# Performance work log

Hardware: AMD Instinct MI355X
Metric: run time of the kernel (lower is better)

## Reference

```python
import jax, jax.numpy as jnp
import numpy as np

T, Q, D, NH, L = 6, 300, 256, 8, 4
DH = D // NH
PC, PT = 2, 1
WT = T - 1
P = PC + WT * PT
DFF = 1024
SHAPES = [(128, 128), (64, 64), (32, 32), (16, 16)]
S_PER_FRAME = sum(h * w for h, w in SHAPES)


def _layer_norm(x, g, b, eps=1e-5):
    mu = jnp.mean(x, -1, keepdims=True)
    v = jnp.mean(jnp.square(x - mu), -1, keepdims=True)
    return (x - mu) * jax.lax.rsqrt(v + eps) * g + b


def _bilinear(vlh, loc, frame_pt, Hl, Wl):
    # vlh: [NH, T*Hl*Wl, DH]; loc: [TQ, NH, P, 2] normalized; frame_pt: np [TQ, P] int32
    x = loc[..., 0] * Wl - 0.5
    y = loc[..., 1] * Hl - 0.5
    x0 = jnp.floor(x)
    y0 = jnp.floor(y)
    fx = x - x0
    fy = y - y0
    x0 = x0.astype(jnp.int32)
    y0 = y0.astype(jnp.int32)
    fbase = (frame_pt[:, None, :] * np.int32(Hl * Wl)).astype(np.int32)  # [TQ,1,P]
    acc = 0.0
    for dy, wy in ((0, 1.0 - fy), (1, fy)):
        for dx, wx in ((0, 1.0 - fx), (1, fx)):
            xi = x0 + dx
            yi = y0 + dy
            ok = (xi >= 0) & (xi < Wl) & (yi >= 0) & (yi < Hl)
            idx = fbase + jnp.clip(yi, 0, Hl - 1) * Wl + jnp.clip(xi, 0, Wl - 1)  # [TQ,NH,P]
            g = jax.vmap(lambda v, i: v[i], in_axes=(0, 1), out_axes=0)(vlh, idx)  # [NH,TQ,P,DH]
            w = wy * wx * ok  # [TQ,NH,P]
            acc = acc + g * jnp.transpose(w, (1, 0, 2))[..., None]
    return acc  # [NH,TQ,P,DH]


def _forward(src, tgt_masks, query_pos, reference_points, src_valid_ratios,
             Wq, bq, Wk, bk, Wv, bv, Wo, bo, norm2_g, norm2_b,
             Wval, bval, Woff, boff, Watt, batt, Wout, bout, norm1_g, norm1_b,
             W1, b1, W2, b2, norm3_g, norm3_b,
             src_spatial_shapes, src_level_start_index):
    shapes = np.asarray(src_spatial_shapes)
    # ---- self-attention across frames (seq=T, batch=Q, as in nn.MultiheadAttention) ----
    qk_in = tgt_masks + query_pos  # [T,Q,D]
    qh = (qk_in @ Wq.T + bq).reshape(T, Q, NH, DH)
    kh = (qk_in @ Wk.T + bk).reshape(T, Q, NH, DH)
    vh = (tgt_masks @ Wv.T + bv).reshape(T, Q, NH, DH)
    logits = jnp.einsum('iqhd,jqhd->qhij', qh, kh) * (1.0 / np.sqrt(DH))
    attn = jax.nn.softmax(logits, -1)
    sa = jnp.einsum('qhij,jqhd->iqhd', attn, vh).reshape(T, Q, D) @ Wo.T + bo
    tgt = _layer_norm(tgt_masks + sa, norm2_g, norm2_b)  # [T,Q,D]

    tgt = tgt.reshape(T * Q, D)
    query = tgt + query_pos.reshape(T * Q, D)

    # ---- current-frame and temporal (same-instance) reference points ----
    ref = reference_points.reshape(T * Q, 2)
    vr0 = src_valid_ratios[0]  # [L,2]
    ref_curr = ref[:, None, :] * vr0[None]  # [TQ,L,2]
    others = np.array([[f for f in range(T) if f != t] for t in range(T)], np.int32)  # [T,WT]
    ref_oth = reference_points[others]  # [T,WT,Q,2]
    ref_oth = jnp.transpose(ref_oth, (0, 2, 1, 3)).reshape(T * Q, WT, 2)
    ref_temp = ref_oth[:, :, None, :] * vr0[None, None]  # [TQ,WT,L,2]

    fid = np.repeat(np.arange(T, dtype=np.int32), Q)  # [TQ]
    oth_fid = np.repeat(others, Q, axis=0)  # [TQ,WT]
    frame_pt = np.concatenate([np.tile(fid[:, None], (1, PC)), oth_fid], axis=1).astype(np.int32)  # [TQ,P]

    # ---- temporal multi-scale deformable cross-attention ----
    value = (src[0] @ Wval.T + bval).reshape(-1, NH, DH)  # [T*S,NH,DH]
    off = (query @ Woff.T + boff).reshape(T * Q, NH, L, P, 2)
    att = jax.nn.softmax((query @ Watt.T + batt).reshape(T * Q, NH, L * P), -1)
    att = att.reshape(T * Q, NH, L, P)

    out = jnp.zeros((T * Q, NH, DH), src.dtype)
    start = 0
    for l in range(L):
        Hl, Wl = int(shapes[l, 0]), int(shapes[l, 1])
        n = T * Hl * Wl
        vlh = value[start:start + n].transpose(1, 0, 2)  # [NH, T*Hl*Wl, DH]
        start += n
        bc = jnp.tile(ref_curr[:, l][:, None, :], (1, PC, 1))  # [TQ,PC,2]
        bt = ref_temp[:, :, l, :]  # [TQ,WT,2]
        base = jnp.concatenate([bc, bt], 1)[:, None]  # [TQ,1,P,2]
        loc = base + off[:, :, l] / jnp.array([Wl, Hl], jnp.float32)  # [TQ,NH,P,2]
        sampled = _bilinear(vlh, loc, frame_pt, Hl, Wl)  # [NH,TQ,P,DH]
        out = out + jnp.einsum('nqpd,qnp->qnd', sampled, att[:, :, l])
    cross = out.reshape(T * Q, D) @ Wout.T + bout
    tgt = _layer_norm(tgt + cross, norm1_g, norm1_b)

    # ---- FFN ----
    h = jax.nn.relu(tgt @ W1.T + b1)
    tgt = _layer_norm(tgt + h @ W2.T + b2, norm3_g, norm3_b)
    return tgt.reshape(T, Q, D)


def setup_inputs() -> dict:
    key = jax.random.key(0)
    ki = iter(jax.random.split(key, 48))

    def rn(shape, s=1.0):
        return jax.random.normal(next(ki), shape, jnp.float32) * s

    return {
        'src': rn((1, T * S_PER_FRAME, D)),
        'tgt_masks': rn((T, Q, D)),
        'query_pos': rn((T, Q, D), 0.5),
        'reference_points': jax.random.uniform(next(ki), (T, Q, 2), jnp.float32, 0.25, 0.75),
        'src_valid_ratios': jax.random.uniform(next(ki), (T, L, 2), jnp.float32, 0.9, 1.0),
        'src_spatial_shapes': jnp.array(SHAPES, jnp.int32),
        'src_level_start_index': jnp.array(np.cumsum([0] + [T * h * w for h, w in SHAPES[:-1]]), jnp.int32),
        'Wq': rn((D, D), 0.02), 'bq': jnp.zeros((D,)),
        'Wk': rn((D, D), 0.02), 'bk': jnp.zeros((D,)),
        'Wv': rn((D, D), 0.02), 'bv': jnp.zeros((D,)),
        'Wo': rn((D, D), 0.02), 'bo': jnp.zeros((D,)),
        'norm2_g': jnp.ones((D,)), 'norm2_b': jnp.zeros((D,)),
        'Wval': rn((D, D), 0.02), 'bval': jnp.zeros((D,)),
        'Woff': rn((NH * L * P * 2, D), 0.01), 'boff': rn((NH * L * P * 2,), 0.1),
        'Watt': rn((NH * L * P, D), 0.01), 'batt': jnp.zeros((NH * L * P,)),
        'Wout': rn((D, D), 0.02), 'bout': jnp.zeros((D,)),
        'norm1_g': jnp.ones((D,)), 'norm1_b': jnp.zeros((D,)),
        'W1': rn((DFF, D), 0.02), 'b1': jnp.zeros((DFF,)),
        'W2': rn((D, DFF), 0.02), 'b2': jnp.zeros((D,)),
        'norm3_g': jnp.ones((D,)), 'norm3_b': jnp.zeros((D,)),
    }


def reference(src, tgt_masks, query_pos, reference_points, src_valid_ratios,
              src_spatial_shapes, src_level_start_index,
              Wq, bq, Wk, bk, Wv, bv, Wo, bo, norm2_g, norm2_b,
              Wval, bval, Woff, boff, Watt, batt, Wout, bout, norm1_g, norm1_b,
              W1, b1, W2, b2, norm3_g, norm3_b):
    return _forward(src, tgt_masks, query_pos, reference_points, src_valid_ratios,
                    Wq, bq, Wk, bk, Wv, bv, Wo, bo, norm2_g, norm2_b,
                    Wval, bval, Woff, boff, Watt, batt, Wout, bout, norm1_g, norm1_b,
                    W1, b1, W2, b2, norm3_g, norm3_b,
                    src_spatial_shapes, src_level_start_index)
```

## Files before the change

kernel.cpp:

```cpp
#include <hip/hip_runtime.h>
#include <hip/hip_bf16.h>

#define T_ 6
#define Q_ 300
#define TQ 1800
#define D_ 256
#define NH_ 8
#define DH_ 32
#define L_ 4
#define P_ 7
#define DFF_ 1024
#define NV 130560
#define VBLK 255

#define OW_VAL 0
#define OW_Q   65536
#define OW_K   131072
#define OW_V   196608
#define OW_O   262144
#define OW_OUT 327680
#define OW_OFF 393216
#define OW_ATT 507904
#define OW_1   565248
#define OW_2   827392
#define OW_TOT 1089536

typedef __attribute__((ext_vector_type(8))) short bf16x8;
typedef __attribute__((ext_vector_type(4))) float f32x4;
typedef __attribute__((ext_vector_type(8))) unsigned short u16x8;
typedef __attribute__((ext_vector_type(4))) unsigned short u16x4;

__device__ inline float bf2f(unsigned short s) {
    union { unsigned u; float f; } v; v.u = ((unsigned)s) << 16;
    return v.f;
}
__device__ inline unsigned short f2b_rn(float f) {
    __hip_bfloat16 h = __float2bfloat16(f);
    union { __hip_bfloat16 h; unsigned short u; } c; c.h = h; return c.u;
}

__global__ __launch_bounds__(256) void wcvt_kernel(
    const float* __restrict__ s0, const float* __restrict__ s1,
    const float* __restrict__ s2, const float* __restrict__ s3,
    const float* __restrict__ s4, const float* __restrict__ s5,
    const float* __restrict__ s6, const float* __restrict__ s7,
    const float* __restrict__ s8, const float* __restrict__ s9,
    unsigned short* __restrict__ dst)
{
    int idx4 = blockIdx.x * blockDim.x + threadIdx.x;
    const int total4 = OW_TOT / 4;
    for (; idx4 < total4; idx4 += gridDim.x * blockDim.x) {
        int e = idx4 * 4;
        const float* s; int off;
        if      (e < OW_Q)   { s = s0; off = e; }
        else if (e < OW_K)   { s = s1; off = e - OW_Q; }
        else if (e < OW_V)   { s = s2; off = e - OW_K; }
        else if (e < OW_O)   { s = s3; off = e - OW_V; }
        else if (e < OW_OUT) { s = s4; off = e - OW_O; }
        else if (e < OW_OFF) { s = s5; off = e - OW_OUT; }
        else if (e < OW_ATT) { s = s6; off = e - OW_OFF; }
        else if (e < OW_1)   { s = s7; off = e - OW_ATT; }
        else if (e < OW_2)   { s = s8; off = e - OW_1; }
        else                 { s = s9; off = e - OW_2; }
        f32x4 v = *(const f32x4*)(s + off);
        u16x4 o;
#pragma unroll
        for (int j = 0; j < 4; j++) o[j] = f2b_rn(v[j]);
        *(u16x4*)(dst + e) = o;
    }
}

__global__ __launch_bounds__(512) void vgemm_kernel(
    const float* __restrict__ A, const unsigned short* __restrict__ wbf,
    const float* __restrict__ bias, unsigned short* __restrict__ out)
{
    __shared__ unsigned short Ws[256 * 256];
    __shared__ float As[2][128 * 32];

    int tid = threadIdx.x;
    int wave = tid >> 6, lane = tid & 63;
    int r = lane & 15, g = lane >> 4;
    int rs = r & 7;
    int base_m = blockIdx.x * 512;

#pragma unroll
    for (int j = 0; j < 16; j++) {
        int o = wave * 16 + j;
        int col = o * 2 + (lane >> 5);
        int slot = lane & 31;
        const unsigned short* s =
            wbf + OW_VAL + (size_t)col * 256 + (size_t)((slot ^ (col & 7)) * 8);
        __builtin_amdgcn_global_load_lds(
            (const __attribute__((address_space(1))) void*)s,
            (__attribute__((address_space(3))) void*)&Ws[o * 512], 16, 0, 0);
    }

#define DMA_A(tile, ks, b) do { \
        int o_ = wave * 2; \
        int ro_ = o_ * 8 + (lane >> 3); \
        int kg_ = (lane & 7) ^ (lane >> 3); \
        const float* s0_ = A + (size_t)(base_m + (tile) * 128 + ro_) * 256 + (ks) * 32 + kg_ * 4; \
        const float* s1_ = s0_ + 8 * 256; \
        __builtin_amdgcn_global_load_lds( \
            (const __attribute__((address_space(1))) void*)s0_, \
            (__attribute__((address_space(3))) void*)&As[b][o_ * 256], 16, 0, 0); \
        __builtin_amdgcn_global_load_lds( \
            (const __attribute__((address_space(1))) void*)s1_, \
            (__attribute__((address_space(3))) void*)&As[b][(o_ + 1) * 256], 16, 0, 0); \
    } while (0)

    DMA_A(0, 0, 0);
    DMA_A(0, 1, 1);

    int wm = wave >> 2, wn = wave & 3;
    f32x4 acc[4][4] = {};

    for (int p = 0; p < 32; ++p) {
        if (p == 31) { asm volatile("s_waitcnt vmcnt(0)" ::: "memory"); }
        else         { asm volatile("s_waitcnt vmcnt(2)" ::: "memory"); }
        __builtin_amdgcn_s_barrier();
        __builtin_amdgcn_sched_barrier(0);

        int tile = p >> 3, ks = p & 7, b = p & 1;

        {
            bf16x8 af[4];
#pragma unroll
            for (int mi = 0; mi < 4; mi++) {
                int row_ = wm * 64 + mi * 16 + r;
                f32x4 lo_ = *(const f32x4*)&As[b][row_ * 32 + (((g * 2) ^ rs) << 2)];
                f32x4 hi_ = *(const f32x4*)&As[b][row_ * 32 + (((g * 2 + 1) ^ rs) << 2)];
#pragma unroll
                for (int j = 0; j < 4; j++) {
                    af[mi][j] = (short)f2b_rn(lo_[j]);
                    af[mi][4 + j] = (short)f2b_rn(hi_[j]);
                }
            }
#pragma unroll
            for (int ni = 0; ni < 4; ni++) {
                int col_ = wn * 64 + ni * 16 + r;
                bf16x8 bfr = *(const bf16x8*)&Ws[col_ * 256 + (((ks * 4 + g) ^ rs) << 3)];
#pragma unroll
                for (int mi = 0; mi < 4; mi++)
                    acc[mi][ni] = __builtin_amdgcn_mfma_f32_16x16x32_bf16(af[mi], bfr, acc[mi][ni], 0, 0, 0);
            }
        }

        __builtin_amdgcn_s_barrier();
        __builtin_amdgcn_sched_barrier(0);

        int pn = p + 2;
        if (pn < 32) DMA_A(pn >> 3, pn & 7, b);

        if (ks == 7) {
            int mbase = base_m + tile * 128 + wm * 64;
#pragma unroll
            for (int ni = 0; ni < 4; ni++) {
                int col = wn * 64 + ni * 16 + r;
                float bv2 = bias[col];
#pragma unroll
                for (int mi = 0; mi < 4; mi++) {
#pragma unroll
                    for (int rr = 0; rr < 4; rr++) {
                        int row = mbase + mi * 16 + g * 4 + rr;
                        out[(size_t)row * 256 + col] = f2b_rn(acc[mi][ni][rr] + bv2);
                    }
                }
            }
#pragma unroll
            for (int mi = 0; mi < 4; mi++)
#pragma unroll
                for (int ni = 0; ni < 4; ni++)
                    acc[mi][ni] = (f32x4){0.f, 0.f, 0.f, 0.f};
        }
    }
#undef DMA_A
}

__global__ __launch_bounds__(256) void attn_wo_ln2_kernel(
    const float* __restrict__ tgtm, const float* __restrict__ qpos,
    const unsigned short* __restrict__ wbf,
    const float* __restrict__ bq, const float* __restrict__ bk,
    const float* __restrict__ bv, const float* __restrict__ bo,
    const float* __restrict__ n2g, const float* __restrict__ n2b,
    float* __restrict__ tgt1, float* __restrict__ query)
{
    int q = blockIdx.x;
    int tid = threadIdx.x;
    __shared__ unsigned short xq[16][264], xv[16][264];
    __shared__ float qs[T_][D_], ks_[T_][D_], vs[T_][D_];
    __shared__ unsigned short po[16][268];
    __shared__ float sa32[16][264];

#pragma unroll
    for (int i = 0; i < T_; i++) {
        size_t base = (size_t)(i * Q_ + q) * D_ + tid;
        float tv = tgtm[base];
        xq[i][tid] = f2b_rn(tv + qpos[base]);
        xv[i][tid] = f2b_rn(tv);
    }
#pragma unroll
    for (int i = T_; i < 16; i++) { xq[i][tid] = 0; xv[i][tid] = 0; }
    __syncthreads();

    int wn = tid >> 6, lane = tid & 63;
    int r = lane & 15, g = lane >> 4;

#pragma unroll
    for (int proj = 0; proj < 3; proj++) {
        const unsigned short* Wp = wbf + (proj == 0 ? OW_Q : (proj == 1 ? OW_K : OW_V));
        const float* bp = (proj == 0) ? bq : (proj == 1) ? bk : bv;
        f32x4 acc[4] = {};
#pragma unroll
        for (int ksx = 0; ksx < 8; ksx++) {
            int kbase = ksx * 32 + g * 8;
            bf16x8 af = (proj == 2) ? *(const bf16x8*)&xv[r][kbase]
                                    : *(const bf16x8*)&xq[r][kbase];
#pragma unroll
            for (int ni = 0; ni < 4; ni++) {
                bf16x8 wf = *(const bf16x8*)&Wp[(size_t)(wn * 64 + ni * 16 + r) * 256 + kbase];
                acc[ni] = __builtin_amdgcn_mfma_f32_16x16x32_bf16(af, wf, acc[ni], 0, 0, 0);
            }
        }
#pragma unroll
        for (int ni = 0; ni < 4; ni++) {
            int col = wn * 64 + ni * 16 + r;
            float bv2 = bp[col];
#pragma unroll
            for (int rr = 0; rr < 4; rr++) {
                int row = g * 4 + rr;
                if (row < T_) {
                    float v = acc[ni][rr] + bv2;
                    if (proj == 0) qs[row][col] = v;
                    else if (proj == 1) ks_[row][col] = v;
                    else vs[row][col] = v;
                }
            }
        }
    }
    __syncthreads();

    const float scale = 0.17677669529663687f;
    float lg[T_][T_];
#pragma unroll
    for (int i = 0; i < T_; i++)
#pragma unroll
        for (int j = 0; j < T_; j++) {
            float p = qs[i][tid] * ks_[j][tid];
#pragma unroll
            for (int m = 16; m >= 1; m >>= 1) p += __shfl_xor(p, m, 32);
            lg[i][j] = p * scale;
        }
#pragma unroll
    for (int i = 0; i < T_; i++) {
        float mx = lg[i][0];
#pragma unroll
        for (int j = 1; j < T_; j++) mx = fmaxf(mx, lg[i][j]);
        float w[T_]; float sum = 0.f;
#pragma unroll
        for (int j = 0; j < T_; j++) { w[j] = __expf(lg[i][j] - mx); sum += w[j]; }
        float inv = 1.f / sum;
        float a = 0.f;
#pragma unroll
        for (int j = 0; j < T_; j++) a += w[j] * inv * vs[j][tid];
        po[i][tid] = f2b_rn(a);
    }
#pragma unroll
    for (int i = T_; i < 16; i++) po[i][tid] = 0;
    __syncthreads();

    const unsigned short* Wo = wbf + OW_O;
    f32x4 acc[4] = {};
#pragma unroll
    for (int ksx = 0; ksx < 8; ksx++) {
        int kbase = ksx * 32 + g * 8;
        bf16x8 af = *(const bf16x8*)&po[r][kbase];
        bf16x8 bfr[4];
#pragma unroll
        for (int ni = 0; ni < 4; ni++)
            bfr[ni] = *(const bf16x8*)&Wo[(size_t)(wn * 64 + ni * 16 + r) * 256 + kbase];
#pragma unroll
        for (int ni = 0; ni < 4; ni++)
            acc[ni] = __builtin_amdgcn_mfma_f32_16x16x32_bf16(af, bfr[ni], acc[ni], 0, 0, 0);
    }
#pragma unroll
    for (int ni = 0; ni < 4; ni++) {
        int col = wn * 64 + ni * 16 + r;
#pragma unroll
        for (int rr = 0; rr < 4; rr++) {
            int row = g * 4 + rr;
            if (row < T_)
                sa32[row][col] = acc[ni][rr] + bo[col] + tgtm[(size_t)(row * Q_ + q) * 256 + col];
        }
    }
    __syncthreads();

    int rl = tid >> 3, l8 = tid & 7;
    if (rl < T_) {
        float s = 0.f, s2 = 0.f;
#pragma unroll
        for (int c = 0; c < 256; c += 8) {
            float v = sa32[rl][c + l8];
            s += v; s2 += v * v;
        }
#pragma unroll
        for (int m = 4; m >= 1; m >>= 1) { s += __shfl_xor(s, m, 64); s2 += __shfl_xor(s2, m, 64); }
        float mu = s * (1.f / 256.f);
        float var = s2 * (1.f / 256.f) - mu * mu;
        float rsv = rsqrtf(var + 1e-5f);
        size_t grow = (size_t)(rl * Q_ + q) * 256;
#pragma unroll
        for (int c = 0; c < 256; c += 8) {
            int cc = c + l8;
            float y = (sa32[rl][cc] - mu) * rsv * n2g[cc] + n2b[cc];
            tgt1[grow + cc] = y;
            query[grow + cc] = y + qpos[grow + cc];
        }
    }
}

__global__ __launch_bounds__(256) void offatt_kernel(
    const float* __restrict__ query, const unsigned short* __restrict__ wbf,
    const float* __restrict__ boff, const float* __restrict__ batt,
    float* __restrict__ offb, float* __restrict__ attl)
{
    int wave = threadIdx.x >> 6;
    int lane = threadIdx.x & 63;
    int wm = wave >> 1, wn = wave & 1;
    int m0 = blockIdx.x * 64 + wm * 32;
    int n0g = blockIdx.y * 64 + wn * 32;
    int seg = (n0g >= 448);
    int n0 = seg ? (n0g - 448) : n0g;
    int Nloc = seg ? 224 : 448;
    const unsigned short* W = wbf + (seg ? OW_ATT : OW_OFF);
    const float* bias = seg ? batt : boff;
    float* out = seg ? attl : offb;
    int r = lane & 15, g = lane >> 4;

    f32x4 acc[2][2] = {};
#pragma unroll
    for (int kk = 0; kk < 256; kk += 32) {
        int kbase = kk + g * 8;
        bf16x8 af[2], wf[2];
#pragma unroll
        for (int mi = 0; mi < 2; mi++) {
            int row = m0 + mi * 16 + r; if (row >= TQ) row = TQ - 1;
            const float* ap = query + (size_t)row * 256 + kbase;
            f32x4 lo = *(const f32x4*)ap, hi = *(const f32x4*)(ap + 4);
#pragma unroll
            for (int j = 0; j < 4; j++) { af[mi][j] = (short)f2b_rn(lo[j]); af[mi][4 + j] = (short)f2b_rn(hi[j]); }
        }
#pragma unroll
        for (int ni = 0; ni < 2; ni++) {
            int col = n0 + ni * 16 + r; if (col >= Nloc) col = Nloc - 1;
            wf[ni] = *(const bf16x8*)&W[(size_t)col * 256 + kbase];
        }
#pragma unroll
        for (int mi = 0; mi < 2; mi++)
#pragma unroll
            for (int ni = 0; ni < 2; ni++)
                acc[mi][ni] = __builtin_amdgcn_mfma_f32_16x16x32_bf16(af[mi], wf[ni], acc[mi][ni], 0, 0, 0);
    }
#pragma unroll
    for (int mi = 0; mi < 2; mi++)
#pragma unroll
        for (int ni = 0; ni < 2; ni++) {
            int col = n0 + ni * 16 + r;
            if (col < Nloc) {
                float bv2 = bias[col];
#pragma unroll
                for (int rr = 0; rr < 4; rr++) {
                    int row = m0 + mi * 16 + g * 4 + rr;
                    if (row < TQ) out[(size_t)row * Nloc + col] = acc[mi][ni][rr] + bv2;
                }
            }
        }
}

__global__ __launch_bounds__(256) void sample_kernel(
    const unsigned short* __restrict__ value, const float* __restrict__ attl,
    const float* __restrict__ off, const float* __restrict__ refp,
    const float* __restrict__ vr, float* __restrict__ out)
{
    int q = blockIdx.x;
    int tid = threadIdx.x;
    int d = tid & 31, h = tid >> 5;
    int t = q / Q_, qq = q - t * Q_;

    __shared__ float aw[NH_][28], ofx[NH_][28], ofy[NH_][28];

    float lgv = (d < 28) ? attl[(size_t)q * 224 + h * 28 + d] : -1e30f;
    float mx = lgv;
#pragma unroll
    for (int m = 16; m >= 1; m >>= 1) mx = fmaxf(mx, __shfl_xor(mx, m, 32));
    float e = (d < 28) ? __expf(lgv - mx) : 0.f;
    float s = e;
#pragma unroll
    for (int m = 16; m >= 1; m >>= 1) s += __shfl_xor(s, m, 32);
    if (d < 28) {
        aw[h][d] = e / s;
        ofx[h][d] = off[(size_t)q * 448 + h * 56 + d * 2 + 0];
        ofy[h][d] = off[(size_t)q * 448 + h * 56 + d * 2 + 1];
    }
    __syncthreads();

    const int WLs[4] = {128, 64, 32, 16};
    const int LST[4] = {0, 98304, 122880, 129024};

    float acc = 0.f;
#pragma unroll
    for (int l = 0; l < L_; l++) {
        const int Wl = WLs[l], Hl = WLs[l];
        const int lst = LST[l];
        float vrx = vr[l * 2 + 0], vry = vr[l * 2 + 1];
#pragma unroll
        for (int p = 0; p < P_; p++) {
            int f = (p < 2) ? t : (((p - 2) < t) ? (p - 2) : (p - 1));
            float rx = refp[(size_t)(f * Q_ + qq) * 2 + 0];
            float ry = refp[(size_t)(f * Q_ + qq) * 2 + 1];
            int ip = l * 7 + p;
            float x = rx * vrx * (float)Wl + ofx[h][ip] - 0.5f;
            float y = ry * vry * (float)Hl + ofy[h][ip] - 0.5f;
            float x0f = floorf(x), y0f = floorf(y);
            float fx = x - x0f, fy = y - y0f;
            int x0 = (int)x0f, y0 = (int)y0f;
            int fbase = lst + f * Hl * Wl;
            float a = aw[h][ip];
#pragma unroll
            for (int dy = 0; dy < 2; dy++) {
// ... 149 lines not shown
        int rl = tid >> 3, l8 = tid & 7;
        int grow = m0 + rl;
        if (grow < TQ) {
            float s = 0.f, s2 = 0.f;
#pragma unroll
            for (int c = 0; c < 256; c += 8) {
                float v = c32[rl][c + l8];
                s += v; s2 += v * v;
            }
#pragma unroll
            for (int m = 4; m >= 1; m >>= 1) { s += __shfl_xor(s, m, 64); s2 += __shfl_xor(s2, m, 64); }
            float mu = s * (1.f / 256.f);
            float var = s2 * (1.f / 256.f) - mu * mu;
            float rs = rsqrtf(var + 1e-5f);
#pragma unroll
            for (int c = 0; c < 256; c += 8) {
                int cc = c + l8;
                dout[(size_t)grow * 256 + cc] = (c32[rl][cc] - mu) * rs * n3g[cc] + n3b[cc];
            }
        }
    }
}

extern "C" void kernel_launch(void* const* d_in, const int* in_sizes, int n_in,
                              void* d_out, int out_size, void* d_ws, size_t ws_size,
                              hipStream_t stream) {
    const float* src  = (const float*)d_in[0];
    const float* tgtm = (const float*)d_in[1];
    const float* qpos = (const float*)d_in[2];
    const float* refp = (const float*)d_in[3];
    const float* vr   = (const float*)d_in[4];
    const float* Wq = (const float*)d_in[7];  const float* bq = (const float*)d_in[8];
    const float* Wk = (const float*)d_in[9];  const float* bk = (const float*)d_in[10];
    const float* Wv = (const float*)d_in[11]; const float* bv = (const float*)d_in[12];
    const float* Wo = (const float*)d_in[13]; const float* bo = (const float*)d_in[14];
    const float* n2g = (const float*)d_in[15]; const float* n2b = (const float*)d_in[16];
    const float* Wval = (const float*)d_in[17]; const float* bval = (const float*)d_in[18];
    const float* Woff = (const float*)d_in[19]; const float* boff = (const float*)d_in[20];
    const float* Watt = (const float*)d_in[21]; const float* batt = (const float*)d_in[22];
    const float* Wout = (const float*)d_in[23]; const float* bout = (const float*)d_in[24];
    const float* n1g = (const float*)d_in[25]; const float* n1b = (const float*)d_in[26];
    const float* W1 = (const float*)d_in[27]; const float* b1 = (const float*)d_in[28];
    const float* W2 = (const float*)d_in[29]; const float* b2 = (const float*)d_in[30];
    const float* n3g = (const float*)d_in[31]; const float* n3b = (const float*)d_in[32];

    char* ws = (char*)d_ws;
    size_t o = 0;
    auto alloc = [&](size_t bytes) -> void* {
        void* p = ws + o; o += (bytes + 255) & ~(size_t)255; return p;
    };
    unsigned short* value = (unsigned short*)alloc((size_t)NV * D_ * 2);
    unsigned short* wbf   = (unsigned short*)alloc((size_t)OW_TOT * 2);
    float* tgt1   = (float*)alloc((size_t)TQ * D_ * 4);
    float* query  = (float*)alloc((size_t)TQ * D_ * 4);
    float* offb   = (float*)alloc((size_t)TQ * 448 * 4);
    float* attl   = (float*)alloc((size_t)TQ * 224 * 4);
    float* samp   = (float*)alloc((size_t)TQ * D_ * 4);

    const int MT = (TQ + 63) / 64;

    wcvt_kernel<<<dim3((OW_TOT / 4 + 255) / 256), dim3(256), 0, stream>>>(
        Wval, Wq, Wk, Wv, Wo, Wout, Woff, Watt, W1, W2, wbf);

    vgemm_kernel<<<dim3(VBLK), dim3(512), 0, stream>>>(src, wbf, bval, value);

    attn_wo_ln2_kernel<<<dim3(Q_), dim3(256), 0, stream>>>(
        tgtm, qpos, wbf, bq, bk, bv, bo, n2g, n2b, tgt1, query);

    offatt_kernel<<<dim3(MT, 11), dim3(256), 0, stream>>>(query, wbf, boff, batt, offb, attl);

    sample_kernel<<<dim3(TQ), dim3(256), 0, stream>>>(value, attl, offb, refp, vr, samp);

    tail_kernel<<<dim3((TQ + 15) / 16), dim3(256), 0, stream>>>(
        samp, wbf, bout, tgt1, n1g, n1b, b1, b2, n3g, n3b, (float*)d_out);
}
```

Before: 183.5 us.

## Fuse offset/attention projection into self-attention kernel and retile value GEMM

The offset and attention-logit projection is folded into the per-query self-attention kernel. The normalized query is kept in shared memory as bf16 instead of being written to and re-read from a global buffer, which removes one launch. The value GEMM is retiled from 255 persistent 512-thread blocks, each holding the full weight matrix in LDS, to 2040 blocks of 256 threads computing 128x128 tiles with double-buffered A and B K-slices. This trades weight reuse for more parallelism and smaller LDS use. Each fused block now computes only 6 real rows in padded 16-row MFMA tiles and reads the offset weights straight from global memory.

```diff
diff --git a/kernel.cpp b/kernel.cpp
--- a/kernel.cpp
+++ b/kernel.cpp
@@ -11,7 +11,6 @@
 #define P_ 7
 #define DFF_ 1024
 #define NV 130560
-#define VBLK 255
 
 #define OW_VAL 0
 #define OW_Q   65536
@@ -70,120 +69,103 @@
     }
 }
 
-__global__ __launch_bounds__(512) void vgemm_kernel(
+__global__ __launch_bounds__(256) void vgemm_kernel(
     const float* __restrict__ A, const unsigned short* __restrict__ wbf,
     const float* __restrict__ bias, unsigned short* __restrict__ out)
 {
-    __shared__ unsigned short Ws[256 * 256];
     __shared__ float As[2][128 * 32];
+    __shared__ unsigned short Bs[2][128 * 32];
 
     int tid = threadIdx.x;
     int wave = tid >> 6, lane = tid & 63;
     int r = lane & 15, g = lane >> 4;
-    int rs = r & 7;
-    int base_m = blockIdx.x * 512;
-
-#pragma unroll
-    for (int j = 0; j < 16; j++) {
-        int o = wave * 16 + j;
-        int col = o * 2 + (lane >> 5);
-        int slot = lane & 31;
-        const unsigned short* s =
-            wbf + OW_VAL + (size_t)col * 256 + (size_t)((slot ^ (col & 7)) * 8);
-        __builtin_amdgcn_global_load_lds(
-            (const __attribute__((address_space(1))) void*)s,
-            (__attribute__((address_space(3))) void*)&Ws[o * 512], 16, 0, 0);
-    }
-
-#define DMA_A(tile, ks, b) do { \
-        int o_ = wave * 2; \
-        int ro_ = o_ * 8 + (lane >> 3); \
-        int kg_ = (lane & 7) ^ (lane >> 3); \
-        const float* s0_ = A + (size_t)(base_m + (tile) * 128 + ro_) * 256 + (ks) * 32 + kg_ * 4; \
-        const float* s1_ = s0_ + 8 * 256; \
-        __builtin_amdgcn_global_load_lds( \
-            (const __attribute__((address_space(1))) void*)s0_, \
-            (__attribute__((address_space(3))) void*)&As[b][o_ * 256], 16, 0, 0); \
-        __builtin_amdgcn_global_load_lds( \
-            (const __attribute__((address_space(1))) void*)s1_, \
-            (__attribute__((address_space(3))) void*)&As[b][(o_ + 1) * 256], 16, 0, 0); \
-    } while (0)
-
-    DMA_A(0, 0, 0);
-    DMA_A(0, 1, 1);
-
-    int wm = wave >> 2, wn = wave & 3;
+    int mt = blockIdx.x >> 1, nh = blockIdx.x & 1;
+    int m0 = mt * 128, n0 = nh * 128;
+    const unsigned short* Wv = wbf + OW_VAL + (size_t)n0 * 256;
+
+#define DMA_A(ks, b) do { \
+        _Pragma("unroll") \
+        for (int j = 0; j < 4; j++) { \
+            int o_ = wave * 4 + j; \
+            int row_ = o_ * 8 + (lane >> 3); \
+            int kg_ = (lane & 7) ^ (lane >> 3); \
+            const float* s_ = A + (size_t)(m0 + row_) * 256 + (ks) * 32 + kg_ * 4; \
+            __builtin_amdgcn_global_load_lds( \
+                (const __attribute__((address_space(1))) void*)s_, \
+                (__attribute__((address_space(3))) void*)&As[b][o_ * 256], 16, 0, 0); \
+        } } while (0)
+
+#define DMA_B(ks, b) do { \
+        _Pragma("unroll") \
+        for (int j = 0; j < 2; j++) { \
+            int o_ = wave * 2 + j; \
+            int col_ = o_ * 16 + (lane >> 2); \
+            int kg_ = (lane & 3) ^ ((lane >> 2) & 3); \
+            const unsigned short* s_ = Wv + (size_t)col_ * 256 + (ks) * 32 + kg_ * 8; \
+            __builtin_amdgcn_global_load_lds( \
+                (const __attribute__((address_space(1))) void*)s_, \
+                (__attribute__((address_space(3))) void*)&Bs[b][o_ * 512], 16, 0, 0); \
+        } } while (0)
+
+    DMA_A(0, 0); DMA_B(0, 0);
+    __syncthreads();
+
+    int wm = wave >> 1, wn = wave & 1;
     f32x4 acc[4][4] = {};
 
-    for (int p = 0; p < 32; ++p) {
-        if (p == 31) { asm volatile("s_waitcnt vmcnt(0)" ::: "memory"); }
-        else         { asm volatile("s_waitcnt vmcnt(2)" ::: "memory"); }
-        __builtin_amdgcn_s_barrier();
-        __builtin_amdgcn_sched_barrier(0);
-
-        int tile = p >> 3, ks = p & 7, b = p & 1;
-
-        {
-            bf16x8 af[4];
-#pragma unroll
-            for (int mi = 0; mi < 4; mi++) {
-                int row_ = wm * 64 + mi * 16 + r;
-                f32x4 lo_ = *(const f32x4*)&As[b][row_ * 32 + (((g * 2) ^ rs) << 2)];
-                f32x4 hi_ = *(const f32x4*)&As[b][row_ * 32 + (((g * 2 + 1) ^ rs) << 2)];
-#pragma unroll
-                for (int j = 0; j < 4; j++) {
-                    af[mi][j] = (short)f2b_rn(lo_[j]);
-                    af[mi][4 + j] = (short)f2b_rn(hi_[j]);
-                }
-            }
-#pragma unroll
-            for (int ni = 0; ni < 4; ni++) {
-                int col_ = wn * 64 + ni * 16 + r;
-                bf16x8 bfr = *(const bf16x8*)&Ws[col_ * 256 + (((ks * 4 + g) ^ rs) << 3)];
-#pragma unroll
-                for (int mi = 0; mi < 4; mi++)
-                    acc[mi][ni] = __builtin_amdgcn_mfma_f32_16x16x32_bf16(af[mi], bfr, acc[mi][ni], 0, 0, 0);
-            }
-        }
-
-        __builtin_amdgcn_s_barrier();
-        __builtin_amdgcn_sched_barrier(0);
-
-        int pn = p + 2;
-        if (pn < 32) DMA_A(pn >> 3, pn & 7, b);
-
-        if (ks == 7) {
-            int mbase = base_m + tile * 128 + wm * 64;
-#pragma unroll
-            for (int ni = 0; ni < 4; ni++) {
-                int col = wn * 64 + ni * 16 + r;
-                float bv2 = bias[col];
-#pragma unroll
-                for (int mi = 0; mi < 4; mi++) {
-#pragma unroll
-                    for (int rr = 0; rr < 4; rr++) {
-                        int row = mbase + mi * 16 + g * 4 + rr;
-                        out[(size_t)row * 256 + col] = f2b_rn(acc[mi][ni][rr] + bv2);
-                    }
-                }
-            }
+#pragma unroll
+    for (int ks = 0; ks < 8; ks++) {
+        int b = ks & 1;
+        if (ks < 7) { DMA_A(ks + 1, b ^ 1); DMA_B(ks + 1, b ^ 1); }
+
+        bf16x8 af[4];
+#pragma unroll
+        for (int mi = 0; mi < 4; mi++) {
+            int row = wm * 64 + mi * 16 + r;
+            f32x4 lo = *(const f32x4*)&As[b][row * 32 + (((g * 2) ^ (r & 7)) << 2)];
+            f32x4 hi = *(const f32x4*)&As[b][row * 32 + (((g * 2 + 1) ^ (r & 7)) << 2)];
+#pragma unroll
+            for (int j = 0; j < 4; j++) {
+                af[mi][j] = (short)f2b_rn(lo[j]);
+                af[mi][4 + j] = (short)f2b_rn(hi[j]);
+            }
+        }
+#pragma unroll
+        for (int ni = 0; ni < 4; ni++) {
+            int col = wn * 64 + ni * 16 + r;
+            bf16x8 bfr = *(const bf16x8*)&Bs[b][col * 32 + ((g ^ (r & 3)) << 3)];
 #pragma unroll
             for (int mi = 0; mi < 4; mi++)
-#pragma unroll
-                for (int ni = 0; ni < 4; ni++)
-                    acc[mi][ni] = (f32x4){0.f, 0.f, 0.f, 0.f};
-        }
+                acc[mi][ni] = __builtin_amdgcn_mfma_f32_16x16x32_bf16(af[mi], bfr, acc[mi][ni], 0, 0, 0);
+        }
+        __syncthreads();
     }
 #undef DMA_A
-}
-
-__global__ __launch_bounds__(256) void attn_wo_ln2_kernel(
+#undef DMA_B
+
+#pragma unroll
+    for (int ni = 0; ni < 4; ni++) {
+        int col = n0 + wn * 64 + ni * 16 + r;
+        float bv2 = bias[col];
+#pragma unroll
+        for (int mi = 0; mi < 4; mi++) {
+#pragma unroll
+            for (int rr = 0; rr < 4; rr++) {
+                int row = m0 + wm * 64 + mi * 16 + g * 4 + rr;
+                out[(size_t)row * 256 + col] = f2b_rn(acc[mi][ni][rr] + bv2);
+            }
+        }
+    }
+}
+
+__global__ __launch_bounds__(256) void attn_offatt_kernel(
     const float* __restrict__ tgtm, const float* __restrict__ qpos,
     const unsigned short* __restrict__ wbf,
     const float* __restrict__ bq, const float* __restrict__ bk,
     const float* __restrict__ bv, const float* __restrict__ bo,
     const float* __restrict__ n2g, const float* __restrict__ n2b,
-    float* __restrict__ tgt1, float* __restrict__ query)
+    const float* __restrict__ boff, const float* __restrict__ batt,
+    float* __restrict__ tgt1, float* __restrict__ offb, float* __restrict__ attl)
 {
     int q = blockIdx.x;
     int tid = threadIdx.x;
@@ -191,6 +173,7 @@
     __shared__ float qs[T_][D_], ks_[T_][D_], vs[T_][D_];
     __shared__ unsigned short po[16][268];
     __shared__ float sa32[16][264];
+    __shared__ unsigned short qb[16][264];
 
 #pragma unroll
     for (int i = 0; i < T_; i++) {
@@ -200,7 +183,7 @@
         xv[i][tid] = f2b_rn(tv);
     }
 #pragma unroll
-    for (int i = T_; i < 16; i++) { xq[i][tid] = 0; xv[i][tid] = 0; }
+    for (int i = T_; i < 16; i++) { xq[i][tid] = 0; xv[i][tid] = 0; qb[i][tid] = 0; }
     __syncthreads();
 
     int wn = tid >> 6, lane = tid & 63;
@@ -270,111 +253,93 @@
     __syncthreads();
 
     const unsigned short* Wo = wbf + OW_O;
-    f32x4 acc[4] = {};
-#pragma unroll
-    for (int ksx = 0; ksx < 8; ksx++) {
-        int kbase = ksx * 32 + g * 8;
-        bf16x8 af = *(const bf16x8*)&po[r][kbase];
-        bf16x8 bfr[4];
-#pragma unroll
-        for (int ni = 0; ni < 4; ni++)
-            bfr[ni] = *(const bf16x8*)&Wo[(size_t)(wn * 64 + ni * 16 + r) * 256 + kbase];
-#pragma unroll
-        for (int ni = 0; ni < 4; ni++)
-            acc[ni] = __builtin_amdgcn_mfma_f32_16x16x32_bf16(af, bfr[ni], acc[ni], 0, 0, 0);
-    }
-#pragma unroll
-    for (int ni = 0; ni < 4; ni++) {
-        int col = wn * 64 + ni * 16 + r;
-#pragma unroll
-        for (int rr = 0; rr < 4; rr++) {
-            int row = g * 4 + rr;
-            if (row < T_)
-                sa32[row][col] = acc[ni][rr] + bo[col] + tgtm[(size_t)(row * Q_ + q) * 256 + col];
-        }
-    }
-    __syncthreads();
-
-    int rl = tid >> 3, l8 = tid & 7;
-    if (rl < T_) {
-        float s = 0.f, s2 = 0.f;
-#pragma unroll
-        for (int c = 0; c < 256; c += 8) {
-            float v = sa32[rl][c + l8];
-            s += v; s2 += v * v;
-        }
-#pragma unroll
-        for (int m = 4; m >= 1; m >>= 1) { s += __shfl_xor(s, m, 64); s2 += __shfl_xor(s2, m, 64); }
-        float mu = s * (1.f / 256.f);
-        float var = s2 * (1.f / 256.f) - mu * mu;
-        float rsv = rsqrtf(var + 1e-5f);
-        size_t grow = (size_t)(rl * Q_ + q) * 256;
-#pragma unroll
-        for (int c = 0; c < 256; c += 8) {
-            int cc = c + l8;
-            float y = (sa32[rl][cc] - mu) * rsv * n2g[cc] + n2b[cc];
-            tgt1[grow + cc] = y;
-            query[grow + cc] = y + qpos[grow + cc];
-        }
-    }
-}
-
-__global__ __launch_bounds__(256) void offatt_kernel(
-    const float* __restrict__ query, const unsigned short* __restrict__ wbf,
-    const float* __restrict__ boff, const float* __restrict__ batt,
-    float* __restrict__ offb, float* __restrict__ attl)
-{
-    int wave = threadIdx.x >> 6;
-    int lane = threadIdx.x & 63;
-    int wm = wave >> 1, wn = wave & 1;
-    int m0 = blockIdx.x * 64 + wm * 32;
-    int n0g = blockIdx.y * 64 + wn * 32;
-    int seg = (n0g >= 448);
-    int n0 = seg ? (n0g - 448) : n0g;
-    int Nloc = seg ? 224 : 448;
-    const unsigned short* W = wbf + (seg ? OW_ATT : OW_OFF);
-    const float* bias = seg ? batt : boff;
-    float* out = seg ? attl : offb;
-    int r = lane & 15, g = lane >> 4;
-
-    f32x4 acc[2][2] = {};
-#pragma unroll
-    for (int kk = 0; kk < 256; kk += 32) {
-        int kbase = kk + g * 8;
-        bf16x8 af[2], wf[2];
-#pragma unroll
-        for (int mi = 0; mi < 2; mi++) {
-            int row = m0 + mi * 16 + r; if (row >= TQ) row = TQ - 1;
-            const float* ap = query + (size_t)row * 256 + kbase;
-            f32x4 lo = *(const f32x4*)ap, hi = *(const f32x4*)(ap + 4);
-#pragma unroll
-            for (int j = 0; j < 4; j++) { af[mi][j] = (short)f2b_rn(lo[j]); af[mi][4 + j] = (short)f2b_rn(hi[j]); }
-        }
-#pragma unroll
-        for (int ni = 0; ni < 2; ni++) {
-            int col = n0 + ni * 16 + r; if (col >= Nloc) col = Nloc - 1;
-            wf[ni] = *(const bf16x8*)&W[(size_t)col * 256 + kbase];
-        }
-#pragma unroll
-        for (int mi = 0; mi < 2; mi++)
-#pragma unroll
-            for (int ni = 0; ni < 2; ni++)
-                acc[mi][ni] = __builtin_amdgcn_mfma_f32_16x16x32_bf16(af[mi], wf[ni], acc[mi][ni], 0, 0, 0);
-    }
-#pragma unroll
-    for (int mi = 0; mi < 2; mi++)
-#pragma unroll
-        for (int ni = 0; ni < 2; ni++) {
-            int col = n0 + ni * 16 + r;
-            if (col < Nloc) {
-                float bv2 = bias[col];
+    {
+        f32x4 acc[4] = {};
+#pragma unroll
+        for (int ksx = 0; ksx < 8; ksx++) {
+            int kbase = ksx * 32 + g * 8;
+            bf16x8 af = *(const bf16x8*)&po[r][kbase];
+#pragma unroll
+            for (int ni = 0; ni < 4; ni++) {
+                bf16x8 bfr = *(const bf16x8*)&Wo[(size_t)(wn * 64 + ni * 16 + r) * 256 + kbase];
+                acc[ni] = __builtin_amdgcn_mfma_f32_16x16x32_bf16(af, bfr, acc[ni], 0, 0, 0);
+            }
+        }
+#pragma unroll
+        for (int ni = 0; ni < 4; ni++) {
+            int col = wn * 64 + ni * 16 + r;
+#pragma unroll
+            for (int rr = 0; rr < 4; rr++) {
+                int row = g * 4 + rr;
+                if (row < T_)
+                    sa32[row][col] = acc[ni][rr] + bo[col] + tgtm[(size_t)(row * Q_ + q) * 256 + col];
+            }
+        }
+    }
+    __syncthreads();
+
+    {
+        int rl = tid >> 3, l8 = tid & 7;
+        if (rl < T_) {
+            float s = 0.f, s2 = 0.f;
+#pragma unroll
+            for (int c = 0; c < 256; c += 8) {
+                float v = sa32[rl][c + l8];
+                s += v; s2 += v * v;
+            }
+#pragma unroll
+            for (int m = 4; m >= 1; m >>= 1) { s += __shfl_xor(s, m, 64); s2 += __shfl_xor(s2, m, 64); }
+            float mu = s * (1.f / 256.f);
+            float var = s2 * (1.f / 256.f) - mu * mu;
+            float rsv = rsqrtf(var + 1e-5f);
+            size_t grow = (size_t)(rl * Q_ + q) * 256;
+#pragma unroll
+            for (int c = 0; c < 256; c += 8) {
+                int cc = c + l8;
+                float y = (sa32[rl][cc] - mu) * rsv * n2g[cc] + n2b[cc];
+                tgt1[grow + cc] = y;
+                qb[rl][cc] = f2b_rn(y + qpos[grow + cc]);
+            }
+        }
+    }
+    __syncthreads();
+
+    {
+        f32x4 acc[11] = {};
+#pragma unroll
+        for (int ksx = 0; ksx < 8; ksx++) {
+            int kbase = ksx * 32 + g * 8;
+            bf16x8 af = *(const bf16x8*)&qb[r][kbase];
+#pragma unroll
+            for (int ni = 0; ni < 11; ni++) {
+                int chunk = wn + 4 * ni;
+                if (chunk < 42) {
+                    const unsigned short* Wrow = (chunk < 28)
+                        ? wbf + OW_OFF + (size_t)(chunk * 16 + r) * 256
+                        : wbf + OW_ATT + (size_t)((chunk - 28) * 16 + r) * 256;
+                    bf16x8 bfr = *(const bf16x8*)&Wrow[kbase];
+                    acc[ni] = __builtin_amdgcn_mfma_f32_16x16x32_bf16(af, bfr, acc[ni], 0, 0, 0);
+                }
+            }
+        }
+#pragma unroll
+        for (int ni = 0; ni < 11; ni++) {
+            int chunk = wn + 4 * ni;
+            if (chunk < 42) {
+                int col = chunk * 16 + r;
+                float bvv = (chunk < 28) ? boff[col] : batt[col - 448];
 #pragma unroll
                 for (int rr = 0; rr < 4; rr++) {
-                    int row = m0 + mi * 16 + g * 4 + rr;
-                    if (row < TQ) out[(size_t)row * Nloc + col] = acc[mi][ni][rr] + bv2;
+                    int row = g * 4 + rr;
+                    if (row < T_) {
+                        size_t gq = (size_t)(row * Q_ + q);
+                        if (chunk < 28) offb[gq * 448 + col] = acc[ni][rr] + bvv;
+                        else            attl[gq * 224 + (col - 448)] = acc[ni][rr] + bvv;
+                    }
                 }
             }
         }
+    }
 }
 
 __global__ __launch_bounds__(256) void sample_kernel(
@@ -630,22 +595,18 @@
     unsigned short* value = (unsigned short*)alloc((size_t)NV * D_ * 2);
     unsigned short* wbf   = (unsigned short*)alloc((size_t)OW_TOT * 2);
     float* tgt1   = (float*)alloc((size_t)TQ * D_ * 4);
-    float* query  = (float*)alloc((size_t)TQ * D_ * 4);
     float* offb   = (float*)alloc((size_t)TQ * 448 * 4);
     float* attl   = (float*)alloc((size_t)TQ * 224 * 4);
     float* samp   = (float*)alloc((size_t)TQ * D_ * 4);
 
-    const int MT = (TQ + 63) / 64;
-
     wcvt_kernel<<<dim3((OW_TOT / 4 + 255) / 256), dim3(256), 0, stream>>>(
         Wval, Wq, Wk, Wv, Wo, Wout, Woff, Watt, W1, W2, wbf);
 
-    vgemm_kernel<<<dim3(VBLK), dim3(512), 0, stream>>>(src, wbf, bval, value);
-
-    attn_wo_ln2_kernel<<<dim3(Q_), dim3(256), 0, stream>>>(
-        tgtm, qpos, wbf, bq, bk, bv, bo, n2g, n2b, tgt1, query);
-
-    offatt_kernel<<<dim3(MT, 11), dim3(256), 0, stream>>>(query, wbf, boff, batt, offb, attl);
+    attn_offatt_kernel<<<dim3(Q_), dim3(256), 0, stream>>>(
+        tgtm, qpos, wbf, bq, bk, bv, bo, n2g, n2b, boff, batt,
+        tgt1, offb, attl);
+
+    vgemm_kernel<<<dim3(2040), dim3(256), 0, stream>>>(src, wbf, bval, value);
 
     sample_kernel<<<dim3(TQ), dim3(256), 0, stream>>>(value, attl, offb, refp, vr, samp);
 
```

Result: slower. 202.6 us (+10.4%).

## Merge value GEMM and self-attention kernels into one heterogeneous launch

Applied to the files above, without the earlier changes.

Fuses the value-projection GEMM and the per-query self-attention/Wo/LayerNorm kernel into a single launch that dispatches on block index, so the two independent stages can run concurrently on the GPU instead of back to back. The attention blocks now run with 512 threads and only use 256 of them, and every block reserves the GEMM's 160KB shared memory footprint. That lowers occupancy for the attention blocks and may serialize them behind the heavy GEMM blocks.

```diff
diff --git a/kernel.cpp b/kernel.cpp
--- a/kernel.cpp
+++ b/kernel.cpp
@@ -70,30 +70,38 @@
     }
 }
 
-__global__ __launch_bounds__(512) void vgemm_kernel(
+__global__ __launch_bounds__(512) void megaA_kernel(
     const float* __restrict__ A, const unsigned short* __restrict__ wbf,
-    const float* __restrict__ bias, unsigned short* __restrict__ out)
+    const float* __restrict__ bias, unsigned short* __restrict__ out,
+    const float* __restrict__ tgtm, const float* __restrict__ qpos,
+    const float* __restrict__ bq, const float* __restrict__ bk,
+    const float* __restrict__ bv, const float* __restrict__ bo,
+    const float* __restrict__ n2g, const float* __restrict__ n2b,
+    float* __restrict__ tgt1, float* __restrict__ query)
 {
-    __shared__ unsigned short Ws[256 * 256];
-    __shared__ float As[2][128 * 32];
+    __shared__ __align__(16) char smem[163840];
 
     int tid = threadIdx.x;
     int wave = tid >> 6, lane = tid & 63;
     int r = lane & 15, g = lane >> 4;
-    int rs = r & 7;
-    int base_m = blockIdx.x * 512;
-
-#pragma unroll
-    for (int j = 0; j < 16; j++) {
-        int o = wave * 16 + j;
-        int col = o * 2 + (lane >> 5);
-        int slot = lane & 31;
-        const unsigned short* s =
-            wbf + OW_VAL + (size_t)col * 256 + (size_t)((slot ^ (col & 7)) * 8);
-        __builtin_amdgcn_global_load_lds(
-            (const __attribute__((address_space(1))) void*)s,
-            (__attribute__((address_space(3))) void*)&Ws[o * 512], 16, 0, 0);
-    }
+
+    if (blockIdx.x < VBLK) {
+        unsigned short* Ws = (unsigned short*)smem;
+        float (*As)[128 * 32] = (float(*)[128 * 32])(smem + 131072);
+        int rs = r & 7;
+        int base_m = blockIdx.x * 512;
+
+#pragma unroll
+        for (int j = 0; j < 16; j++) {
+            int o = wave * 16 + j;
+            int col = o * 2 + (lane >> 5);
+            int slot = lane & 31;
+            const unsigned short* s =
+                wbf + OW_VAL + (size_t)col * 256 + (size_t)((slot ^ (col & 7)) * 8);
+            __builtin_amdgcn_global_load_lds(
+                (const __attribute__((address_space(1))) void*)s,
+                (__attribute__((address_space(3))) void*)&Ws[o * 512], 16, 0, 0);
+        }
 
 #define DMA_A(tile, ks, b) do { \
         int o_ = wave * 2; \
@@ -109,212 +117,215 @@
             (__attribute__((address_space(3))) void*)&As[b][(o_ + 1) * 256], 16, 0, 0); \
     } while (0)
 
-    DMA_A(0, 0, 0);
-    DMA_A(0, 1, 1);
-
-    int wm = wave >> 2, wn = wave & 3;
-    f32x4 acc[4][4] = {};
-
-    for (int p = 0; p < 32; ++p) {
-        if (p == 31) { asm volatile("s_waitcnt vmcnt(0)" ::: "memory"); }
-        else         { asm volatile("s_waitcnt vmcnt(2)" ::: "memory"); }
-        __builtin_amdgcn_s_barrier();
-        __builtin_amdgcn_sched_barrier(0);
-
-        int tile = p >> 3, ks = p & 7, b = p & 1;
-
-        {
-            bf16x8 af[4];
-#pragma unroll
-            for (int mi = 0; mi < 4; mi++) {
-                int row_ = wm * 64 + mi * 16 + r;
-                f32x4 lo_ = *(const f32x4*)&As[b][row_ * 32 + (((g * 2) ^ rs) << 2)];
-                f32x4 hi_ = *(const f32x4*)&As[b][row_ * 32 + (((g * 2 + 1) ^ rs) << 2)];
-#pragma unroll
-                for (int j = 0; j < 4; j++) {
-                    af[mi][j] = (short)f2b_rn(lo_[j]);
-                    af[mi][4 + j] = (short)f2b_rn(hi_[j]);
-                }
-            }
-#pragma unroll
-            for (int ni = 0; ni < 4; ni++) {
-                int col_ = wn * 64 + ni * 16 + r;
-                bf16x8 bfr = *(const bf16x8*)&Ws[col_ * 256 + (((ks * 4 + g) ^ rs) << 3)];
+        DMA_A(0, 0, 0);
+        DMA_A(0, 1, 1);
+
+        int wm = wave >> 2, wn = wave & 3;
+        f32x4 acc[4][4] = {};
+
+        for (int p = 0; p < 32; ++p) {
+            if (p == 31) { asm volatile("s_waitcnt vmcnt(0)" ::: "memory"); }
+            else         { asm volatile("s_waitcnt vmcnt(2)" ::: "memory"); }
+            __builtin_amdgcn_s_barrier();
+            __builtin_amdgcn_sched_barrier(0);
+
+            int tile = p >> 3, ks = p & 7, b = p & 1;
+
+            {
+                bf16x8 af[4];
+#pragma unroll
+                for (int mi = 0; mi < 4; mi++) {
+                    int row_ = wm * 64 + mi * 16 + r;
+                    f32x4 lo_ = *(const f32x4*)&As[b][row_ * 32 + (((g * 2) ^ rs) << 2)];
+                    f32x4 hi_ = *(const f32x4*)&As[b][row_ * 32 + (((g * 2 + 1) ^ rs) << 2)];
+#pragma unroll
+                    for (int j = 0; j < 4; j++) {
+                        af[mi][j] = (short)f2b_rn(lo_[j]);
+                        af[mi][4 + j] = (short)f2b_rn(hi_[j]);
+                    }
+                }
+#pragma unroll
+                for (int ni = 0; ni < 4; ni++) {
+                    int col_ = wn * 64 + ni * 16 + r;
+                    bf16x8 bfr = *(const bf16x8*)&Ws[col_ * 256 + (((ks * 4 + g) ^ rs) << 3)];
+#pragma unroll
+                    for (int mi = 0; mi < 4; mi++)
+                        acc[mi][ni] = __builtin_amdgcn_mfma_f32_16x16x32_bf16(af[mi], bfr, acc[mi][ni], 0, 0, 0);
+                }
+            }
+
+            __builtin_amdgcn_s_barrier();
+            __builtin_amdgcn_sched_barrier(0);
+
+            int pn = p + 2;
+            if (pn < 32) DMA_A(pn >> 3, pn & 7, b);
+
+            if (ks == 7) {
+                int mbase = base_m + tile * 128 + wm * 64;
+#pragma unroll
+                for (int ni = 0; ni < 4; ni++) {
+                    int col = wn * 64 + ni * 16 + r;
+                    float bv2 = bias[col];
+#pragma unroll
+                    for (int mi = 0; mi < 4; mi++) {
+#pragma unroll
+                        for (int rr = 0; rr < 4; rr++) {
+                            int row = mbase + mi * 16 + g * 4 + rr;
+                            out[(size_t)row * 256 + col] = f2b_rn(acc[mi][ni][rr] + bv2);
+                        }
+                    }
+                }
 #pragma unroll
                 for (int mi = 0; mi < 4; mi++)
-                    acc[mi][ni] = __builtin_amdgcn_mfma_f32_16x16x32_bf16(af[mi], bfr, acc[mi][ni], 0, 0, 0);
-            }
-        }
-
-        __builtin_amdgcn_s_barrier();
-        __builtin_amdgcn_sched_barrier(0);
-
-        int pn = p + 2;
-        if (pn < 32) DMA_A(pn >> 3, pn & 7, b);
-
-        if (ks == 7) {
-            int mbase = base_m + tile * 128 + wm * 64;
+#pragma unroll
+                    for (int ni = 0; ni < 4; ni++)
+                        acc[mi][ni] = (f32x4){0.f, 0.f, 0.f, 0.f};
+            }
+        }
+#undef DMA_A
+    } else {
+        int q = blockIdx.x - VBLK;
+        auto xq   = (unsigned short(*)[264])(smem);
+        auto xv   = (unsigned short(*)[264])(smem + 8448);
+        auto qs   = (float(*)[256])(smem + 16896);
+        auto ks_  = (float(*)[256])(smem + 23040);
+        auto vs   = (float(*)[256])(smem + 29184);
+        auto po   = (unsigned short(*)[268])(smem + 35328);
+        auto sa32 = (float(*)[264])(smem + 43904);
+
+        bool act = (tid < 256);
+
+        if (act) {
+#pragma unroll
+            for (int i = 0; i < T_; i++) {
+                size_t base = (size_t)(i * Q_ + q) * D_ + tid;
+                float tv = tgtm[base];
+                xq[i][tid] = f2b_rn(tv + qpos[base]);
+                xv[i][tid] = f2b_rn(tv);
+            }
+#pragma unroll
+            for (int i = T_; i < 16; i++) { xq[i][tid] = 0; xv[i][tid] = 0; }
+        }
+        __syncthreads();
+
+        int wn = tid >> 6;
+
+        if (act) {
+#pragma unroll
+            for (int proj = 0; proj < 3; proj++) {
+                const unsigned short* Wp = wbf + (proj == 0 ? OW_Q : (proj == 1 ? OW_K : OW_V));
+                const float* bp = (proj == 0) ? bq : (proj == 1) ? bk : bv;
+                f32x4 acc[4] = {};
+#pragma unroll
+                for (int ksx = 0; ksx < 8; ksx++) {
+                    int kbase = ksx * 32 + g * 8;
+                    bf16x8 af = (proj == 2) ? *(const bf16x8*)&xv[r][kbase]
+                                            : *(const bf16x8*)&xq[r][kbase];
+#pragma unroll
+                    for (int ni = 0; ni < 4; ni++) {
+                        bf16x8 wf = *(const bf16x8*)&Wp[(size_t)(wn * 64 + ni * 16 + r) * 256 + kbase];
+                        acc[ni] = __builtin_amdgcn_mfma_f32_16x16x32_bf16(af, wf, acc[ni], 0, 0, 0);
+                    }
+                }
+#pragma unroll
+                for (int ni = 0; ni < 4; ni++) {
+                    int col = wn * 64 + ni * 16 + r;
+                    float bv2 = bp[col];
+#pragma unroll
+                    for (int rr = 0; rr < 4; rr++) {
+                        int row = g * 4 + rr;
+                        if (row < T_) {
+                            float v = acc[ni][rr] + bv2;
+                            if (proj == 0) qs[row][col] = v;
+                            else if (proj == 1) ks_[row][col] = v;
+                            else vs[row][col] = v;
+                        }
+                    }
+                }
+            }
+        }
+        __syncthreads();
+
+        if (act) {
+            const float scale = 0.17677669529663687f;
+            float lg[T_][T_];
+#pragma unroll
+            for (int i = 0; i < T_; i++)
+#pragma unroll
+                for (int j = 0; j < T_; j++) {
+                    float p = qs[i][tid] * ks_[j][tid];
+#pragma unroll
+                    for (int m = 16; m >= 1; m >>= 1) p += __shfl_xor(p, m, 32);
+                    lg[i][j] = p * scale;
+                }
+#pragma unroll
+            for (int i = 0; i < T_; i++) {
+                float mx = lg[i][0];
+#pragma unroll
+                for (int j = 1; j < T_; j++) mx = fmaxf(mx, lg[i][j]);
+                float w[T_]; float sum = 0.f;
+#pragma unroll
+                for (int j = 0; j < T_; j++) { w[j] = __expf(lg[i][j] - mx); sum += w[j]; }
+                float inv = 1.f / sum;
+                float a = 0.f;
+#pragma unroll
+                for (int j = 0; j < T_; j++) a += w[j] * inv * vs[j][tid];
+                po[i][tid] = f2b_rn(a);
+            }
+#pragma unroll
+            for (int i = T_; i < 16; i++) po[i][tid] = 0;
+        }
+        __syncthreads();
+
+        if (act) {
+            const unsigned short* Wo = wbf + OW_O;
+            f32x4 acc[4] = {};
+#pragma unroll
+            for (int ksx = 0; ksx < 8; ksx++) {
+                int kbase = ksx * 32 + g * 8;
+                bf16x8 af = *(const bf16x8*)&po[r][kbase];
+#pragma unroll
+                for (int ni = 0; ni < 4; ni++) {
+                    bf16x8 bfr = *(const bf16x8*)&Wo[(size_t)(wn * 64 + ni * 16 + r) * 256 + kbase];
+                    acc[ni] = __builtin_amdgcn_mfma_f32_16x16x32_bf16(af, bfr, acc[ni], 0, 0, 0);
+                }
+            }
 #pragma unroll
             for (int ni = 0; ni < 4; ni++) {
                 int col = wn * 64 + ni * 16 + r;
-                float bv2 = bias[col];
-#pragma unroll
-                for (int mi = 0; mi < 4; mi++) {
-#pragma unroll
-                    for (int rr = 0; rr < 4; rr++) {
-                        int row = mbase + mi * 16 + g * 4 + rr;
-                        out[(size_t)row * 256 + col] = f2b_rn(acc[mi][ni][rr] + bv2);
-                    }
-                }
-            }
-#pragma unroll
-            for (int mi = 0; mi < 4; mi++)
-#pragma unroll
-                for (int ni = 0; ni < 4; ni++)
-                    acc[mi][ni] = (f32x4){0.f, 0.f, 0.f, 0.f};
-        }
-    }
-#undef DMA_A
-}
-
-__global__ __launch_bounds__(256) void attn_wo_ln2_kernel(
-    const float* __restrict__ tgtm, const float* __restrict__ qpos,
-    const unsigned short* __restrict__ wbf,
-    const float* __restrict__ bq, const float* __restrict__ bk,
-    const float* __restrict__ bv, const float* __restrict__ bo,
-    const float* __restrict__ n2g, const float* __restrict__ n2b,
-    float* __restrict__ tgt1, float* __restrict__ query)
-{
-    int q = blockIdx.x;
-    int tid = threadIdx.x;
-    __shared__ unsigned short xq[16][264], xv[16][264];
-    __shared__ float qs[T_][D_], ks_[T_][D_], vs[T_][D_];
-    __shared__ unsigned short po[16][268];
-    __shared__ float sa32[16][264];
-
-#pragma unroll
-    for (int i = 0; i < T_; i++) {
-        size_t base = (size_t)(i * Q_ + q) * D_ + tid;
-        float tv = tgtm[base];
-        xq[i][tid] = f2b_rn(tv + qpos[base]);
-        xv[i][tid] = f2b_rn(tv);
-    }
-#pragma unroll
-    for (int i = T_; i < 16; i++) { xq[i][tid] = 0; xv[i][tid] = 0; }
-    __syncthreads();
-
-    int wn = tid >> 6, lane = tid & 63;
-    int r = lane & 15, g = lane >> 4;
-
-#pragma unroll
-    for (int proj = 0; proj < 3; proj++) {
-        const unsigned short* Wp = wbf + (proj == 0 ? OW_Q : (proj == 1 ? OW_K : OW_V));
-        const float* bp = (proj == 0) ? bq : (proj == 1) ? bk : bv;
-        f32x4 acc[4] = {};
-#pragma unroll
-        for (int ksx = 0; ksx < 8; ksx++) {
-            int kbase = ksx * 32 + g * 8;
-            bf16x8 af = (proj == 2) ? *(const bf16x8*)&xv[r][kbase]
-                                    : *(const bf16x8*)&xq[r][kbase];
-#pragma unroll
-            for (int ni = 0; ni < 4; ni++) {
-                bf16x8 wf = *(const bf16x8*)&Wp[(size_t)(wn * 64 + ni * 16 + r) * 256 + kbase];
-                acc[ni] = __builtin_amdgcn_mfma_f32_16x16x32_bf16(af, wf, acc[ni], 0, 0, 0);
-            }
-        }
-#pragma unroll
-        for (int ni = 0; ni < 4; ni++) {
-            int col = wn * 64 + ni * 16 + r;
-            float bv2 = bp[col];
-#pragma unroll
-            for (int rr = 0; rr < 4; rr++) {
-                int row = g * 4 + rr;
-                if (row < T_) {
-                    float v = acc[ni][rr] + bv2;
-                    if (proj == 0) qs[row][col] = v;
-                    else if (proj == 1) ks_[row][col] = v;
-                    else vs[row][col] = v;
-                }
-            }
-        }
-    }
-    __syncthreads();
-
-    const float scale = 0.17677669529663687f;
-    float lg[T_][T_];
-#pragma unroll
-    for (int i = 0; i < T_; i++)
-#pragma unroll
-        for (int j = 0; j < T_; j++) {
-            float p = qs[i][tid] * ks_[j][tid];
-#pragma unroll
-            for (int m = 16; m >= 1; m >>= 1) p += __shfl_xor(p, m, 32);
-            lg[i][j] = p * scale;
-        }
-#pragma unroll
-    for (int i = 0; i < T_; i++) {
-        float mx = lg[i][0];
-#pragma unroll
-        for (int j = 1; j < T_; j++) mx = fmaxf(mx, lg[i][j]);
-        float w[T_]; float sum = 0.f;
-#pragma unroll
-        for (int j = 0; j < T_; j++) { w[j] = __expf(lg[i][j] - mx); sum += w[j]; }
-        float inv = 1.f / sum;
-        float a = 0.f;
-#pragma unroll
-        for (int j = 0; j < T_; j++) a += w[j] * inv * vs[j][tid];
-        po[i][tid] = f2b_rn(a);
-    }
-#pragma unroll
-    for (int i = T_; i < 16; i++) po[i][tid] = 0;
-    __syncthreads();
-
-    const unsigned short* Wo = wbf + OW_O;
-    f32x4 acc[4] = {};
-#pragma unroll
-    for (int ksx = 0; ksx < 8; ksx++) {
-        int kbase = ksx * 32 + g * 8;
-        bf16x8 af = *(const bf16x8*)&po[r][kbase];
-        bf16x8 bfr[4];
-#pragma unroll
-        for (int ni = 0; ni < 4; ni++)
-            bfr[ni] = *(const bf16x8*)&Wo[(size_t)(wn * 64 + ni * 16 + r) * 256 + kbase];
-#pragma unroll
-        for (int ni = 0; ni < 4; ni++)
-            acc[ni] = __builtin_amdgcn_mfma_f32_16x16x32_bf16(af, bfr[ni], acc[ni], 0, 0, 0);
-    }
-#pragma unroll
-    for (int ni = 0; ni < 4; ni++) {
-        int col = wn * 64 + ni * 16 + r;
-#pragma unroll
-        for (int rr = 0; rr < 4; rr++) {
-            int row = g * 4 + rr;
-            if (row < T_)
-                sa32[row][col] = acc[ni][rr] + bo[col] + tgtm[(size_t)(row * Q_ + q) * 256 + col];
-        }
-    }
-    __syncthreads();
-
-    int rl = tid >> 3, l8 = tid & 7;
-    if (rl < T_) {
-        float s = 0.f, s2 = 0.f;
-#pragma unroll
-        for (int c = 0; c < 256; c += 8) {
-            float v = sa32[rl][c + l8];
-            s += v; s2 += v * v;
-        }
-#pragma unroll
-        for (int m = 4; m >= 1; m >>= 1) { s += __shfl_xor(s, m, 64); s2 += __shfl_xor(s2, m, 64); }
-        float mu = s * (1.f / 256.f);
-        float var = s2 * (1.f / 256.f) - mu * mu;
-        float rsv = rsqrtf(var + 1e-5f);
-        size_t grow = (size_t)(rl * Q_ + q) * 256;
-#pragma unroll
-        for (int c = 0; c < 256; c += 8) {
-            int cc = c + l8;
-            float y = (sa32[rl][cc] - mu) * rsv * n2g[cc] + n2b[cc];
-            tgt1[grow + cc] = y;
-            query[grow + cc] = y + qpos[grow + cc];
+#pragma unroll
+                for (int rr = 0; rr < 4; rr++) {
+                    int row = g * 4 + rr;
+                    if (row < T_)
+                        sa32[row][col] = acc[ni][rr] + bo[col] + tgtm[(size_t)(row * Q_ + q) * 256 + col];
+                }
+            }
+        }
+        __syncthreads();
+
+        if (tid < 128) {
+            int rl = tid >> 3, l8 = tid & 7;
+            if (rl < T_) {
+                float s = 0.f, s2 = 0.f;
+#pragma unroll
+                for (int c = 0; c < 256; c += 8) {
+                    float v = sa32[rl][c + l8];
+                    s += v; s2 += v * v;
+                }
+#pragma unroll
+                for (int m = 4; m >= 1; m >>= 1) { s += __shfl_xor(s, m, 64); s2 += __shfl_xor(s2, m, 64); }
+                float mu = s * (1.f / 256.f);
+                float var = s2 * (1.f / 256.f) - mu * mu;
+                float rsv = rsqrtf(var + 1e-5f);
+                size_t grow = (size_t)(rl * Q_ + q) * 256;
+#pragma unroll
+                for (int c = 0; c < 256; c += 8) {
+                    int cc = c + l8;
+                    float y = (sa32[rl][cc] - mu) * rsv * n2g[cc] + n2b[cc];
+                    tgt1[grow + cc] = y;
+                    query[grow + cc] = y + qpos[grow + cc];
+                }
+            }
         }
     }
 }
@@ -640,10 +651,9 @@
     wcvt_kernel<<<dim3((OW_TOT / 4 + 255) / 256), dim3(256), 0, stream>>>(
         Wval, Wq, Wk, Wv, Wo, Wout, Woff, Watt, W1, W2, wbf);
 
-    vgemm_kernel<<<dim3(VBLK), dim3(512), 0, stream>>>(src, wbf, bval, value);
-
-    attn_wo_ln2_kernel<<<dim3(Q_), dim3(256), 0, stream>>>(
-        tgtm, qpos, wbf, bq, bk, bv, bo, n2g, n2b, tgt1, query);
+    megaA_kernel<<<dim3(VBLK + Q_), dim3(512), 0, stream>>>(
+        src, wbf, bval, value,
+        tgtm, qpos, bq, bk, bv, bo, n2g, n2b, tgt1, query);
 
     offatt_kernel<<<dim3(MT, 11), dim3(256), 0, stream>>>(query, wbf, boff, batt, offb, attl);
 
```

Result: no change. 186.7 us (+1.8%).
